# Optimization experiments

Hardware: AMD Instinct MI355X
Metric: run time of the kernel (lower is better)

The kernel has to match this reference:

```python
import jax, jax.numpy as jnp
import numpy as np

N = 20000        # nodes per type
E = 320000       # edges per type (avg degree 16)
H = 8            # heads
F0 = 128         # initial feature dim
F_UNI = 256      # n_unified
F_OUT = 64       # n_units per layer
N_USER = 20000   # shape_ret[0]
N_CLASSES = 2


def setup_inputs() -> dict:
    key = jax.random.key(0)
    ks = jax.random.split(key, 32)
    nrm = lambda k, s: jax.random.normal(k, s, dtype=jnp.float32) * 0.05
    inp = {
        "hemb0": nrm(ks[0], (N, F0)),
        "hemb1": nrm(ks[1], (N, F0)),
        "W0": nrm(ks[2], (F0, F_UNI)),
        "W1": nrm(ks[3], (F0, F_UNI)),
    }
    i = 4
    for t in range(2):
        for l, fin in enumerate([F_UNI, H * F_OUT]):
            inp[f"g{t}l{l}_w"] = nrm(ks[i], (H, fin, F_OUT)); i += 1
            inp[f"g{t}l{l}_asrc"] = nrm(ks[i], (H, F_OUT)); i += 1
            inp[f"g{t}l{l}_atrg"] = nrm(ks[i], (H, F_OUT)); i += 1
    inp["aw1"] = nrm(ks[i], (F_UNI, F_OUT)); i += 1
    inp["aw2"] = nrm(ks[i], (F_OUT, F_OUT)); i += 1
    inp["am"] = nrm(ks[i], (F_OUT,)); i += 1
    inp["fc_w"] = nrm(ks[i], (F_OUT * 3, N_CLASSES)); i += 1
    inp["fc_b"] = jnp.zeros((N_CLASSES,), jnp.float32); i += 1
    inp["edge0"] = jax.random.randint(ks[i], (2, E), 0, N, dtype=jnp.int32); i += 1
    inp["edge1"] = jax.random.randint(ks[i], (2, E), 0, N, dtype=jnp.int32)
    return inp


def spgat(h, src, trg, w, asrc, atrg):
    """Sparse GAT layer: h [N,f_in], edge list src/trg [E] -> [N,H,f_out]."""
    n = h.shape[0]
    hp = jnp.einsum('nf,hfo->hno', h, w)              # [H,N,O]
    s = jnp.einsum('hno,ho->nh', hp, asrc)            # [N,H]
    t = jnp.einsum('hno,ho->nh', hp, atrg)            # [N,H]
    e = jax.nn.leaky_relu(s[src] + t[trg], negative_slope=0.2)  # [E,H]
    ex = jnp.exp(e - jnp.max(e))                      # global max shift (as in source)
    denom = jax.ops.segment_sum(ex, trg, num_segments=n)[trg] + 1e-16
    alpha = ex / denom                                # [E,H]
    msg = jnp.transpose(hp, (1, 0, 2))[src] * alpha[:, :, None]  # [E,H,O]
    return jax.ops.segment_sum(msg, trg, num_segments=n)         # [N,H,O]


def reference(hemb0, hemb1, W0, W1,
              g0l0_w, g0l0_asrc, g0l0_atrg, g0l1_w, g0l1_asrc, g0l1_atrg,
              g1l0_w, g1l0_asrc, g1l0_atrg, g1l1_w, g1l1_asrc, g1l1_atrg,
              aw1, aw2, am, fc_w, fc_b, edge0, edge1):
    trans0 = hemb0 @ W0                                # [N,F_UNI]
    trans1 = hemb1 @ W1
    stacks = [
        (trans0, edge0, (g0l0_w, g0l0_asrc, g0l0_atrg), (g0l1_w, g0l1_asrc, g0l1_atrg)),
        (trans1, edge1, (g1l0_w, g1l0_asrc, g1l0_atrg), (g1l1_w, g1l1_asrc, g1l1_atrg)),
    ]
    heter = []
    for trans, edge, p0, p1 in stacks:
        src, trg = edge[0], edge[1]
        x = spgat(trans, src, trg, *p0)                # [N,H,F_OUT]
        x = jax.nn.elu(x.reshape(N, -1))               # [N,H*F_OUT]
        x = spgat(x, src, trg, *p1).mean(axis=1)       # [N,F_OUT]
        heter.append(x[:N_USER][:, None, :])
    type_aware = jnp.concatenate(heter, axis=1)        # [N_USER, 2, F_OUT]
    # faithful to source: feature = trans_emb[0] where trans_emb is the LAST
    # type's transformed embedding -> row 0, shape [F_UNI], broadcast over nodes
    feature = trans1[0]
    q = jnp.tanh(feature @ aw1 + type_aware @ aw2)     # [N_USER,2,F_OUT]
    beta = jax.nn.softmax(q @ am, axis=-1)             # [N_USER,2]
    fusion = jnp.einsum('nr,nrd->nd', beta, type_aware)[:, None, :]
    ret = jnp.concatenate([type_aware, fusion], axis=1).reshape(N_USER, -1)
    return jax.nn.log_softmax(ret @ fc_w + fc_b, axis=-1)   # [N_USER, 2]
```

## Files before the change

### kernel.cpp

```cpp
#include <hip/hip_runtime.h>
#include <hip/hip_bf16.h>


typedef __hip_bfloat16 bf16;
typedef __attribute__((ext_vector_type(8))) short short8;
typedef __attribute__((ext_vector_type(4))) float f32x4;

__device__ __forceinline__ float bf2f(bf16 v) { return __bfloat162float(v); }
__device__ __forceinline__ float ldin(const void* p, long i, int f32) {
  return f32 ? ((const float*)p)[i] : bf2f(((const bf16*)p)[i]);
}
__device__ __forceinline__ short f2bfbits(float f) {
  bf16 h = __float2bfloat16(f);
  return *reinterpret_cast<short*>(&h);
}
__device__ __forceinline__ float bfbits2f(short b) {
  unsigned u = ((unsigned)(unsigned short)b) << 16;
  return __uint_as_float(u);
}

__global__ __launch_bounds__(64) void detect_kernel(const void* __restrict__ x,
                                                    int* __restrict__ flag) {
  int tid = threadIdx.x;
  float m = 0.f;
  for (int i = tid; i < 2048; i += 64) {
    float v = fabsf(bf2f(((const bf16*)x)[i]));
    if (!(v <= 1e3f)) v = 1e9f;
    m = fmaxf(m, v);
  }
#pragma unroll
  for (int off = 32; off; off >>= 1) m = fmaxf(m, __shfl_xor(m, off));
  if (tid == 0) flag[0] = (m > 1e3f) ? 1 : 0;
}

#define GBM 128
#define GBN 64
#define GBK 64

__device__ __forceinline__ int swz(int row, int kbyte) {
  return row * 128 + (kbyte ^ ((row & 7) << 4));
}

__global__ __launch_bounds__(256) void gemm_mfma(const void* __restrict__ A, int amode,
                                                 const void* __restrict__ B, int bmode,
                                                 bf16* __restrict__ C,
                                                 int M, int K, int Nc,
                                                 const int* __restrict__ flag) {
  __shared__ bf16 As[GBM * GBK];
  __shared__ bf16 Bs[GBN * GBK];
  const int f32 = flag[0];
  const int af32 = (amode == 1) ? f32 : 0;
  const int m0 = blockIdx.x * GBM;
  const int n0 = blockIdx.y * GBN;
  const int tid = threadIdx.x;
  const int lane = tid & 63;
  const int wrow = (tid >> 6) * 32;

  f32x4 acc[2][4];
#pragma unroll
  for (int m = 0; m < 2; m++)
#pragma unroll
    for (int n = 0; n < 4; n++)
#pragma unroll
      for (int r = 0; r < 4; r++) acc[m][n][r] = 0.f;

  for (int kt = 0; kt < K; kt += GBK) {
#pragma unroll
    for (int j = 0; j < 4; j++) {
      int idx = tid + j * 256;
      int row = idx >> 3;
      int ks = idx & 7;
      int gm = m0 + row;
      short8 v;
#pragma unroll
      for (int e = 0; e < 8; e++) v[e] = 0;
      if (gm < M) {
        long base = (long)gm * K + kt + ks * 8;
        if (!af32) {
          v = *(const short8*)((const bf16*)A + base);
        } else {
          const float* Af = (const float*)A + base;
#pragma unroll
          for (int e = 0; e < 8; e++) v[e] = f2bfbits(Af[e]);
        }
      }
      *(short8*)((char*)As + swz(row, ks * 16)) = v;
    }
    {
      int n = tid & 63;
      int ks0 = tid >> 6;
#pragma unroll
      for (int jj = 0; jj < 2; jj++) {
        int ks = ks0 + jj * 4;
        int k = kt + ks * 8;
        int col = n0 + n;
        long base;
        int cstr;
        if (bmode == 0) { base = (long)k * Nc + col; cstr = Nc; }
        else { base = ((long)(col >> 6) * K + k) * 64 + (col & 63); cstr = 64; }
        short8 v;
        if (f32) {
          const float* Bf = (const float*)B;
#pragma unroll
          for (int e = 0; e < 8; e++) v[e] = f2bfbits(Bf[base + (long)e * cstr]);
        } else {
          const bf16* Bh = (const bf16*)B;
#pragma unroll
          for (int e = 0; e < 8; e++) v[e] = *(const short*)&Bh[base + (long)e * cstr];
        }
        *(short8*)((char*)Bs + swz(n, ks * 16)) = v;
      }
    }
    __syncthreads();
#pragma unroll
    for (int kh = 0; kh < 2; kh++) {
      int klane = kh * 64 + ((lane >> 4) << 4);
      short8 af[2], bfr[4];
#pragma unroll
      for (int m = 0; m < 2; m++) {
        int row = wrow + m * 16 + (lane & 15);
        af[m] = *(const short8*)((const char*)As + swz(row, klane));
      }
#pragma unroll
      for (int n = 0; n < 4; n++) {
        int col = n * 16 + (lane & 15);
        bfr[n] = *(const short8*)((const char*)Bs + swz(col, klane));
      }
#pragma unroll
      for (int m = 0; m < 2; m++)
#pragma unroll
        for (int n = 0; n < 4; n++)
          acc[m][n] = __builtin_amdgcn_mfma_f32_16x16x32_bf16(af[m], bfr[n], acc[m][n], 0, 0, 0);
    }
    __syncthreads();
  }
#pragma unroll
  for (int m = 0; m < 2; m++) {
#pragma unroll
    for (int r = 0; r < 4; r++) {
      int row = m0 + wrow + m * 16 + ((lane >> 4) << 2) + r;
      if (row < M) {
#pragma unroll
        for (int n = 0; n < 4; n++) {
          int col = n0 + n * 16 + (lane & 15);
          C[(long)row * Nc + col] = __float2bfloat16(acc[m][n][r]);
        }
      }
    }
  }
}

__global__ __launch_bounds__(256) void st_kernel(const bf16* __restrict__ hp,
                                                 const void* __restrict__ asrc,
                                                 const void* __restrict__ atrg,
                                                 float* __restrict__ sv,
                                                 float* __restrict__ tv, int N,
                                                 const int* __restrict__ flag) {
  const int f32 = flag[0];
  int i = blockIdx.x * 256 + threadIdx.x;
  if (i >= N * 8) return;
  int h = i / N;
  int n = i - h * N;
  const bf16* hpp = hp + (long)n * 512 + h * 64;
  float s = 0.f, t = 0.f;
#pragma unroll
  for (int c = 0; c < 8; c++) {
    short8 v = *(const short8*)(hpp + c * 8);
#pragma unroll
    for (int e = 0; e < 8; e++) {
      float x = bfbits2f(v[e]);
      int o = c * 8 + e;
      s += x * ldin(asrc, h * 64 + o, f32);
      t += x * ldin(atrg, h * 64 + o, f32);
    }
  }
  sv[n * 8 + h] = s;
  tv[n * 8 + h] = t;
}

__global__ void hist_kernel(const int* __restrict__ trg, int* __restrict__ deg, int E) {
  int e = blockIdx.x * 256 + threadIdx.x;
  if (e < E) atomicAdd(&deg[trg[e]], 1);
}

__global__ __launch_bounds__(1024) void scan_kernel(const int* __restrict__ deg,
                                                    int* __restrict__ row_ptr,
                                                    int* __restrict__ fil, int N) {
  __shared__ int sums[1024];
  int tid = threadIdx.x;
  int chunk = (N + 1023) >> 10;
  int start = tid * chunk;
  int end = start + chunk;
  if (start > N) start = N;
  if (end > N) end = N;
  int s = 0;
  for (int i = start; i < end; i++) s += deg[i];
  sums[tid] = s;
  __syncthreads();
  for (int off = 1; off < 1024; off <<= 1) {
    int add = (tid >= off) ? sums[tid - off] : 0;
    __syncthreads();
    sums[tid] += add;
    __syncthreads();
  }
  int run = (tid > 0) ? sums[tid - 1] : 0;
  for (int i = start; i < end; i++) {
    row_ptr[i] = run;
    fil[i] = run;
    run += deg[i];
  }
  if (tid == 0) row_ptr[N] = sums[1023];
}

__global__ void fill_kernel(const int* __restrict__ src, const int* __restrict__ trg,
                            int* __restrict__ fil, int* __restrict__ col, int E) {
  int e = blockIdx.x * 256 + threadIdx.x;
  if (e >= E) return;
  int t = trg[e];
  int pos = atomicAdd(&fil[t], 1);
  col[pos] = src[e];
}

__device__ __forceinline__ float exleaky(float v) {
  v = v > 0.f ? v : 0.2f * v;
  return __expf(v);
}

__global__ __launch_bounds__(256) void aggregate(const bf16* __restrict__ hp,
                                                 const float* __restrict__ sv,
                                                 const float* __restrict__ tv,
                                                 const int* __restrict__ row_ptr,
                                                 const int* __restrict__ col_src,
                                                 void* __restrict__ out, int N, int mode) {
  const int wid = threadIdx.x >> 6;
  const int lane = threadIdx.x & 63;
  const int n = blockIdx.x * 4 + wid;
  if (n >= N) return;
  const int start = row_ptr[n];
  const int deg = row_ptr[n + 1] - start;
  const int h = lane >> 3;
  const float tvh = tv[(long)n * 8 + h];
  const bf16* __restrict__ hpc = hp + lane * 8;

  float acc[8] = {0.f, 0.f, 0.f, 0.f, 0.f, 0.f, 0.f, 0.f};
  float den = 1e-16f;

  for (int base = 0; base < deg; base += 64) {
    int cnt = deg - base;
    if (cnt > 64) cnt = 64;
    int mysrc = (lane < cnt) ? col_src[start + base + lane] : 0;
    int e = 0;
    for (; e + 4 <= cnt; e += 4) {
      int s0 = __shfl(mysrc, e + 0);
      int s1 = __shfl(mysrc, e + 1);
      int s2 = __shfl(mysrc, e + 2);
      int s3 = __shfl(mysrc, e + 3);
      short8 v0 = *(const short8*)(hpc + (long)s0 * 512);
      short8 v1 = *(const short8*)(hpc + (long)s1 * 512);
      short8 v2 = *(const short8*)(hpc + (long)s2 * 512);
      short8 v3 = *(const short8*)(hpc + (long)s3 * 512);
      float a0 = exleaky(sv[(long)s0 * 8 + h] + tvh);
      float a1 = exleaky(sv[(long)s1 * 8 + h] + tvh);
      float a2 = exleaky(sv[(long)s2 * 8 + h] + tvh);
      float a3 = exleaky(sv[(long)s3 * 8 + h] + tvh);
      den += a0 + a1 + a2 + a3;
#pragma unroll
      for (int j = 0; j < 8; j++) acc[j] += a0 * bfbits2f(v0[j]);
#pragma unroll
      for (int j = 0; j < 8; j++) acc[j] += a1 * bfbits2f(v1[j]);
#pragma unroll
      for (int j = 0; j < 8; j++) acc[j] += a2 * bfbits2f(v2[j]);
#pragma unroll
      for (int j = 0; j < 8; j++) acc[j] += a3 * bfbits2f(v3[j]);
    }
    for (; e < cnt; e++) {
      int s0 = __shfl(mysrc, e);
      short8 v0 = *(const short8*)(hpc + (long)s0 * 512);
      float a0 = exleaky(sv[(long)s0 * 8 + h] + tvh);
      den += a0;
#pragma unroll
      for (int j = 0; j < 8; j++) acc[j] += a0 * bfbits2f(v0[j]);
    }
  }

  const float dinv = 1.f / den;
  if (mode == 0) {
    short8 o8;
#pragma unroll
    for (int j = 0; j < 8; j++) {
      float s = acc[j] * dinv;
      float ev = s > 0.f ? s : expm1f(s);
      o8[j] = f2bfbits(ev);
    }
    *(short8*)((bf16*)out + (long)n * 512 + lane * 8) = o8;
  } else {
    float r[8];
#pragma unroll
    for (int j = 0; j < 8; j++) r[j] = acc[j] * dinv;
#pragma unroll
    for (int m = 8; m <= 32; m <<= 1)
#pragma unroll
      for (int j = 0; j < 8; j++) r[j] += __shfl_xor(r[j], m);
    if (lane < 8) {
      float* o = (float*)out + (long)n * 128 + lane * 8;
#pragma unroll
      for (int j = 0; j < 8; j++) o[j] = r[j] * 0.125f;
    }
  }
}

__global__ __launch_bounds__(64) void favec_kernel(const bf16* __restrict__ trans1,
                                                   const void* __restrict__ aw1,
                                                   float* __restrict__ favec,
                                                   const int* __restrict__ flag) {
  const int f32 = flag[0];
  int o = threadIdx.x;
  float acc = 0.f;
  for (int k = 0; k < 256; k++) acc += bf2f(trans1[k]) * ldin(aw1, k * 64 + o, f32);
  favec[o] = acc;
}

__global__ __launch_bounds__(64) void final_kernel(const float* __restrict__ ta,
                                                   const float* __restrict__ favec,
                                                   const void* __restrict__ aw2,
                                                   const void* __restrict__ am,
                                                   const void* __restrict__ fcw,
                                                   const void* __restrict__ fcb,
                                                   void* __restrict__ out, int N,
                                                   const int* __restrict__ flag) {
  const int f32 = flag[0];
  int n = blockIdx.x;
  int o = threadIdx.x;
  __shared__ float s0[64], s1[64];
  float ta0 = ta[(long)n * 128 + o];
  float ta1 = ta[(long)n * 128 + 64 + o];
  s0[o] = ta0;
  s1[o] = ta1;
  __syncthreads();
  float f = favec[o];
  float acc0 = f, acc1 = f;
  for (int k = 0; k < 64; k++) {
    float w = ldin(aw2, k * 64 + o, f32);
    acc0 += s0[k] * w;
    acc1 += s1[k] * w;
  }
  float amv = ldin(am, o, f32);
  float p0 = tanhf(acc0) * amv;
  float p1 = tanhf(acc1) * amv;
#pragma unroll
  for (int off = 32; off > 0; off >>= 1) {
    p0 += __shfl_xor(p0, off);
    p1 += __shfl_xor(p1, off);
  }
  float mx = fmaxf(p0, p1);
  float e0 = __expf(p0 - mx), e1 = __expf(p1 - mx);
  float b0 = e0 / (e0 + e1), b1 = e1 / (e0 + e1);
  float fus = b0 * ta0 + b1 * ta1;
  float l0 = ta0 * ldin(fcw, o * 2 + 0, f32) + ta1 * ldin(fcw, (64 + o) * 2 + 0, f32) +
             fus * ldin(fcw, (128 + o) * 2 + 0, f32);
  float l1 = ta0 * ldin(fcw, o * 2 + 1, f32) + ta1 * ldin(fcw, (64 + o) * 2 + 1, f32) +
             fus * ldin(fcw, (128 + o) * 2 + 1, f32);
#pragma unroll
  for (int off = 32; off > 0; off >>= 1) {
    l0 += __shfl_xor(l0, off);
    l1 += __shfl_xor(l1, off);
  }
  if (o == 0) {
    l0 += ldin(fcb, 0, f32);
    l1 += ldin(fcb, 1, f32);
    float m2 = fmaxf(l0, l1);
    float lse = m2 + logf(__expf(l0 - m2) + __expf(l1 - m2));
    if (f32) {
      ((float*)out)[n * 2 + 0] = l0 - lse;
      ((float*)out)[n * 2 + 1] = l1 - lse;
    } else {
      ((bf16*)out)[n * 2 + 0] = __float2bfloat16(l0 - lse);
      ((bf16*)out)[n * 2 + 1] = __float2bfloat16(l1 - lse);
    }
  }
}

extern "C" void kernel_launch(void* const* d_in, const int* in_sizes, int n_in,
                              void* d_out, int out_size, void* d_ws, size_t ws_size,
                              hipStream_t stream) {
  constexpr int N = 20000, E = 320000, H = 8, F0 = 128, FU = 256, FO = 64;
  const void* hemb[2] = {d_in[0], d_in[1]};
  const void* W[2] = {d_in[2], d_in[3]};
  const void* gw[2][2] = {{d_in[4], d_in[7]}, {d_in[10], d_in[13]}};
  const void* gasrc[2][2] = {{d_in[5], d_in[8]}, {d_in[11], d_in[14]}};
  const void* gatrg[2][2] = {{d_in[6], d_in[9]}, {d_in[12], d_in[15]}};
  const void* aw1 = d_in[16];
  const void* aw2 = d_in[17];
  const void* am = d_in[18];
  const void* fcw = d_in[19];
  const void* fcb = d_in[20];
  const int* edge[2] = {(const int*)d_in[21], (const int*)d_in[22]};

  char* p = (char*)d_ws;
  auto alloc = [&](size_t bytes) -> void* {
    void* r = (void*)p;
    p += (bytes + 255) & ~(size_t)255;
    return r;
  };
  int* flag = (int*)alloc(4);
  bf16* trans = (bf16*)alloc((size_t)N * FU * 2);
  bf16* hp = (bf16*)alloc((size_t)N * H * FO * 2);
  bf16* xbuf = (bf16*)alloc((size_t)N * H * FO * 2);
  float* sv = (float*)alloc((size_t)N * H * 4);
  float* tv = (float*)alloc((size_t)N * H * 4);
  float* ta = (float*)alloc((size_t)N * 2 * FO * 4);
  float* favec = (float*)alloc(FO * 4);
  int* deg[2];
  int* rp[2];
  int* fil[2];
  int* col[2];
  for (int t = 0; t < 2; t++) {
    deg[t] = (int*)alloc((size_t)N * 4);
    rp[t] = (int*)alloc((size_t)(N + 1) * 4);
    fil[t] = (int*)alloc((size_t)N * 4);
    col[t] = (int*)alloc((size_t)E * 4);
  }

  detect_kernel<<<1, 64, 0, stream>>>(hemb[0], flag);

  for (int t = 0; t < 2; t++) {
    hipMemsetAsync(deg[t], 0, (size_t)N * 4, stream);
    hist_kernel<<<(E + 255) / 256, 256, 0, stream>>>(edge[t] + E, deg[t], E);
    scan_kernel<<<1, 1024, 0, stream>>>(deg[t], rp[t], fil[t], N);
    fill_kernel<<<(E + 255) / 256, 256, 0, stream>>>(edge[t], edge[t] + E, fil[t], col[t], E);
  }

  const int gmx = (N + GBM - 1) / GBM;
  const int gagg = (N + 3) / 4;

  for (int t = 0; t < 2; t++) {
    gemm_mfma<<<dim3(gmx, FU / GBN), 256, 0, stream>>>(hemb[t], 1, W[t], 0, trans,
                                                       N, F0, FU, flag);
    gemm_mfma<<<dim3(gmx, (H * FO) / GBN), 256, 0, stream>>>(trans, 0, gw[t][0], 1, hp,
                                                             N, FU, H * FO, flag);
    st_kernel<<<(N * H + 255) / 256, 256, 0, stream>>>(hp, gasrc[t][0], gatrg[t][0], sv, tv, N, flag);
    aggregate<<<gagg, 256, 0, stream>>>(hp, sv, tv, rp[t], col[t], xbuf, N, 0);
    gemm_mfma<<<dim3(gmx, (H * FO) / GBN), 256, 0, stream>>>(xbuf, 0, gw[t][1], 1, hp,
                                                             N, H * FO, H * FO, flag);
    st_kernel<<<(N * H + 255) / 256, 256, 0, stream>>>(hp, gasrc[t][1], gatrg[t][1], sv, tv, N, flag);
    aggregate<<<gagg, 256, 0, stream>>>(hp, sv, tv, rp[t], col[t], ta + t * FO, N, 1);
  }

  favec_kernel<<<1, 64, 0, stream>>>(trans, aw1, favec, flag);
  final_kernel<<<N, 64, 0, stream>>>(ta, favec, aw2, am, fcw, fcb, d_out, N, flag);
}
```

Baseline: 660.8 us.

## Fuse attention score dot products into GEMM epilogue and software-pipeline aggregation loads

Computes the per-node, per-head source and target attention scores inside the GEMM epilogue. Each block's 64-column tile is one head, so the scores come straight from the fp32 accumulators using shuffle reductions. This removes the separate st_kernel launch and its re-read of hp. The aggregate inner loop is also restructured to prefetch the next group of four neighbor rows while accumulating the current group, which raises memory-level parallelism at the cost of more registers.

```diff
diff --git a/kernel.cpp b/kernel.cpp
--- a/kernel.cpp
+++ b/kernel.cpp
@@ -45,6 +45,10 @@
                                                  const void* __restrict__ B, int bmode,
                                                  bf16* __restrict__ C,
                                                  int M, int K, int Nc,
+                                                 const void* __restrict__ stasrc,
+                                                 const void* __restrict__ statrg,
+                                                 float* __restrict__ svp,
+                                                 float* __restrict__ tvp,
                                                  const int* __restrict__ flag) {
   __shared__ bf16 As[GBM * GBK];
   __shared__ bf16 Bs[GBN * GBK];
@@ -134,6 +138,38 @@
     }
     __syncthreads();
   }
+  if (svp) {
+    const int h = blockIdx.y;
+    const int cl = lane & 15;
+    float av[4], bv[4];
+#pragma unroll
+    for (int n = 0; n < 4; n++) {
+      av[n] = ldin(stasrc, h * 64 + n * 16 + cl, f32);
+      bv[n] = ldin(statrg, h * 64 + n * 16 + cl, f32);
+    }
+#pragma unroll
+    for (int m = 0; m < 2; m++) {
+#pragma unroll
+      for (int r = 0; r < 4; r++) {
+        float s = 0.f, t = 0.f;
+#pragma unroll
+        for (int n = 0; n < 4; n++) {
+          s += acc[m][n][r] * av[n];
+          t += acc[m][n][r] * bv[n];
+        }
+#pragma unroll
+        for (int off = 1; off <= 8; off <<= 1) {
+          s += __shfl_xor(s, off);
+          t += __shfl_xor(t, off);
+        }
+        int row = m0 + wrow + m * 16 + ((lane >> 4) << 2) + r;
+        if (cl == 0 && row < M) {
+          svp[(long)row * 8 + h] = s;
+          tvp[(long)row * 8 + h] = t;
+        }
+      }
+    }
+  }
 #pragma unroll
   for (int m = 0; m < 2; m++) {
 #pragma unroll
@@ -148,34 +184,6 @@
       }
     }
   }
-}
-
-__global__ __launch_bounds__(256) void st_kernel(const bf16* __restrict__ hp,
-                                                 const void* __restrict__ asrc,
-                                                 const void* __restrict__ atrg,
-                                                 float* __restrict__ sv,
-                                                 float* __restrict__ tv, int N,
-                                                 const int* __restrict__ flag) {
-  const int f32 = flag[0];
-  int i = blockIdx.x * 256 + threadIdx.x;
-  if (i >= N * 8) return;
-  int h = i / N;
-  int n = i - h * N;
-  const bf16* hpp = hp + (long)n * 512 + h * 64;
-  float s = 0.f, t = 0.f;
-#pragma unroll
-  for (int c = 0; c < 8; c++) {
-    short8 v = *(const short8*)(hpp + c * 8);
-#pragma unroll
-    for (int e = 0; e < 8; e++) {
-      float x = bfbits2f(v[e]);
-      int o = c * 8 + e;
-      s += x * ldin(asrc, h * 64 + o, f32);
-      t += x * ldin(atrg, h * 64 + o, f32);
-    }
-  }
-  sv[n * 8 + h] = s;
-  tv[n * 8 + h] = t;
 }
 
 __global__ void hist_kernel(const int* __restrict__ trg, int* __restrict__ deg, int E) {
@@ -245,41 +253,54 @@
   float acc[8] = {0.f, 0.f, 0.f, 0.f, 0.f, 0.f, 0.f, 0.f};
   float den = 1e-16f;
 
+#define AG_LOAD(E, V0, V1, V2, V3, Q0, Q1, Q2, Q3)                  \
+  {                                                                 \
+    int t0 = __shfl(mysrc, (E) + 0), t1 = __shfl(mysrc, (E) + 1);   \
+    int t2 = __shfl(mysrc, (E) + 2), t3 = __shfl(mysrc, (E) + 3);   \
+    V0 = *(const short8*)(hpc + (long)t0 * 512);                    \
+    V1 = *(const short8*)(hpc + (long)t1 * 512);                    \
+    V2 = *(const short8*)(hpc + (long)t2 * 512);                    \
+    V3 = *(const short8*)(hpc + (long)t3 * 512);                    \
+    Q0 = sv[(long)t0 * 8 + h];                                      \
+    Q1 = sv[(long)t1 * 8 + h];                                      \
+    Q2 = sv[(long)t2 * 8 + h];                                      \
+    Q3 = sv[(long)t3 * 8 + h];                                      \
+  }
+#define AG_ACC(V0, V1, V2, V3, Q0, Q1, Q2, Q3)                      \
+  {                                                                 \
+    float a0 = exleaky(Q0 + tvh), a1 = exleaky(Q1 + tvh);           \
+    float a2 = exleaky(Q2 + tvh), a3 = exleaky(Q3 + tvh);           \
+    den += a0 + a1 + a2 + a3;                                       \
+    _Pragma("unroll")                                               \
+    for (int j = 0; j < 8; j++)                                     \
+      acc[j] += a0 * bfbits2f(V0[j]) + a1 * bfbits2f(V1[j]) +       \
+                a2 * bfbits2f(V2[j]) + a3 * bfbits2f(V3[j]);        \
+  }
+
   for (int base = 0; base < deg; base += 64) {
     int cnt = deg - base;
     if (cnt > 64) cnt = 64;
     int mysrc = (lane < cnt) ? col_src[start + base + lane] : 0;
-    int e = 0;
-    for (; e + 4 <= cnt; e += 4) {
-      int s0 = __shfl(mysrc, e + 0);
-      int s1 = __shfl(mysrc, e + 1);
-      int s2 = __shfl(mysrc, e + 2);
-      int s3 = __shfl(mysrc, e + 3);
-      short8 v0 = *(const short8*)(hpc + (long)s0 * 512);
-      short8 v1 = *(const short8*)(hpc + (long)s1 * 512);
-      short8 v2 = *(const short8*)(hpc + (long)s2 * 512);
-      short8 v3 = *(const short8*)(hpc + (long)s3 * 512);
-      float a0 = exleaky(sv[(long)s0 * 8 + h] + tvh);
-      float a1 = exleaky(sv[(long)s1 * 8 + h] + tvh);
-      float a2 = exleaky(sv[(long)s2 * 8 + h] + tvh);
-      float a3 = exleaky(sv[(long)s3 * 8 + h] + tvh);
-      den += a0 + a1 + a2 + a3;
-#pragma unroll
-      for (int j = 0; j < 8; j++) acc[j] += a0 * bfbits2f(v0[j]);
-#pragma unroll
-      for (int j = 0; j < 8; j++) acc[j] += a1 * bfbits2f(v1[j]);
-#pragma unroll
-      for (int j = 0; j < 8; j++) acc[j] += a2 * bfbits2f(v2[j]);
-#pragma unroll
-      for (int j = 0; j < 8; j++) acc[j] += a3 * bfbits2f(v3[j]);
-    }
-    for (; e < cnt; e++) {
+    int nfull = cnt & ~3;
+    if (nfull) {
+      short8 v0, v1, v2, v3;
+      float q0, q1, q2, q3;
+      AG_LOAD(0, v0, v1, v2, v3, q0, q1, q2, q3);
+      for (int e = 4; e < nfull; e += 4) {
+        short8 w0 = v0, w1 = v1, w2 = v2, w3 = v3;
+        float p0 = q0, p1 = q1, p2 = q2, p3 = q3;
+        AG_LOAD(e, v0, v1, v2, v3, q0, q1, q2, q3);
+        AG_ACC(w0, w1, w2, w3, p0, p1, p2, p3);
+      }
+      AG_ACC(v0, v1, v2, v3, q0, q1, q2, q3);
+    }
+    for (int e = nfull; e < cnt; e++) {
       int s0 = __shfl(mysrc, e);
-      short8 v0 = *(const short8*)(hpc + (long)s0 * 512);
-      float a0 = exleaky(sv[(long)s0 * 8 + h] + tvh);
-      den += a0;
-#pragma unroll
-      for (int j = 0; j < 8; j++) acc[j] += a0 * bfbits2f(v0[j]);
+      short8 v = *(const short8*)(hpc + (long)s0 * 512);
+      float a = exleaky(sv[(long)s0 * 8 + h] + tvh);
+      den += a;
+#pragma unroll
+      for (int j = 0; j < 8; j++) acc[j] += a * bfbits2f(v[j]);
     }
   }
 
@@ -435,14 +456,15 @@
 
   for (int t = 0; t < 2; t++) {
     gemm_mfma<<<dim3(gmx, FU / GBN), 256, 0, stream>>>(hemb[t], 1, W[t], 0, trans,
-                                                       N, F0, FU, flag);
+                                                       N, F0, FU,
+                                                       nullptr, nullptr, nullptr, nullptr, flag);
     gemm_mfma<<<dim3(gmx, (H * FO) / GBN), 256, 0, stream>>>(trans, 0, gw[t][0], 1, hp,
-                                                             N, FU, H * FO, flag);
-    st_kernel<<<(N * H + 255) / 256, 256, 0, stream>>>(hp, gasrc[t][0], gatrg[t][0], sv, tv, N, flag);
+                                                             N, FU, H * FO,
+                                                             gasrc[t][0], gatrg[t][0], sv, tv, flag);
     aggregate<<<gagg, 256, 0, stream>>>(hp, sv, tv, rp[t], col[t], xbuf, N, 0);
     gemm_mfma<<<dim3(gmx, (H * FO) / GBN), 256, 0, stream>>>(xbuf, 0, gw[t][1], 1, hp,
-                                                             N, H * FO, H * FO, flag);
-    st_kernel<<<(N * H + 255) / 256, 256, 0, stream>>>(hp, gasrc[t][1], gatrg[t][1], sv, tv, N, flag);
+                                                             N, H * FO, H * FO,
+                                                             gasrc[t][1], gatrg[t][1], sv, tv, flag);
     aggregate<<<gagg, 256, 0, stream>>>(hp, sv, tv, rp[t], col[t], ta + t * FO, N, 1);
   }
 
```

Measured after the change: 626.5 us. 1.05x faster.
